# Optimization experiments

Hardware: AMD Instinct MI355X
Metric: run time of the kernel (lower is better)

## Reference

```python
import jax, jax.numpy as jnp
import numpy as np
from jax import lax

K = 3
K2 = K * K
EPS = 1e-5


def conv3x3(x, w, b=None):
    # x [B,C,H,W], w [O,C,3,3], padding=1, stride=1
    out = lax.conv_general_dilated(x, w, (1, 1), [(1, 1), (1, 1)],
                                   dimension_numbers=('NCHW', 'OIHW', 'NCHW'))
    if b is not None:
        out = out + b[None, :, None, None]
    return out


def deform_conv(x, w_off, b_off, w_mod, b_mod, w):
    # DCNv2-style deformable conv, k=3, stride=1, pad=1, dilation=1, no bias.
    B, C, H, W = x.shape
    O = w.shape[0]
    off = conv3x3(x, w_off, b_off).reshape(B, K2, 2, H, W)   # (dy,dx) per tap
    mod = 2.0 * jax.nn.sigmoid(conv3x3(x, w_mod, b_mod))      # [B,9,H,W]
    dy, dx = off[:, :, 0], off[:, :, 1]

    ky = (jnp.arange(K) - 1).astype(x.dtype)
    base_y = jnp.repeat(ky, K)   # [9]
    base_x = jnp.tile(ky, K)     # [9]
    ii = jnp.arange(H, dtype=x.dtype)[:, None]
    jj = jnp.arange(W, dtype=x.dtype)[None, :]
    py = ii[None, None] + base_y[None, :, None, None] + dy   # [B,9,H,W]
    px = jj[None, None] + base_x[None, :, None, None] + dx

    def sample(xb, pyb, pxb):
        # xb [C,H,W]; pyb/pxb [9,H,W] -> [C,9,H,W], bilinear w/ zero pad
        y0 = jnp.floor(pyb)
        x0 = jnp.floor(pxb)
        wy = pyb - y0
        wx = pxb - x0
        flat = xb.reshape(C, -1)
        acc = jnp.zeros((C, K2, H, W), xb.dtype)
        for yc, xc, wt in ((y0, x0, (1 - wy) * (1 - wx)),
                           (y0, x0 + 1, (1 - wy) * wx),
                           (y0 + 1, x0, wy * (1 - wx)),
                           (y0 + 1, x0 + 1, wy * wx)):
            yi = yc.astype(jnp.int32)
            xi = xc.astype(jnp.int32)
            valid = (yi >= 0) & (yi < H) & (xi >= 0) & (xi < W)
            idx = (jnp.clip(yi, 0, H - 1) * W + jnp.clip(xi, 0, W - 1)).reshape(-1)
            g = jnp.take(flat, idx, axis=1).reshape(C, K2, H, W)
            acc = acc + g * (wt * valid)[None]
        return acc

    patches = jax.vmap(sample)(x, py, px)          # [B,C,9,H,W]
    patches = patches * mod[:, None]               # modulated
    return jnp.einsum('bckhw,ock->bohw', patches, w.reshape(O, C, K2))


def bn_relu(x):
    # BatchNorm2d(affine=False), train-mode batch stats, biased variance
    mean = jnp.mean(x, axis=(0, 2, 3), keepdims=True)
    var = jnp.mean(jnp.square(x - mean), axis=(0, 2, 3), keepdims=True)
    return jax.nn.relu((x - mean) * lax.rsqrt(var + EPS))


def maxpool2(x):
    return lax.reduce_window(x, -jnp.inf, lax.max, (1, 1, 2, 2), (1, 1, 2, 2), 'VALID')


def setup_inputs() -> dict:
    key = jax.random.key(0)
    ks = jax.random.split(key, 11)
    B, Cin, Cout, H, W = 4, 64, 128, 128, 128
    std1 = 1.0 / np.sqrt(Cin * K2)
    std2 = 1.0 / np.sqrt(Cout * K2)
    return {
        'x': jax.random.normal(ks[0], (B, Cin, H, W), jnp.float32),
        'w_off1': jax.random.normal(ks[1], (2 * K2, Cin, K, K), jnp.float32) * 0.01,
        'b_off1': jax.random.normal(ks[2], (2 * K2,), jnp.float32) * 0.01,
        'w_mod1': jax.random.normal(ks[3], (K2, Cin, K, K), jnp.float32) * 0.01,
        'b_mod1': jnp.zeros((K2,), jnp.float32),
        'w1': jax.random.normal(ks[4], (Cout, Cin, K, K), jnp.float32) * std1,
        'w_off2': jax.random.normal(ks[5], (2 * K2, Cout, K, K), jnp.float32) * 0.01,
        'b_off2': jax.random.normal(ks[6], (2 * K2,), jnp.float32) * 0.01,
        'w_mod2': jax.random.normal(ks[7], (K2, Cout, K, K), jnp.float32) * 0.01,
        'b_mod2': jnp.zeros((K2,), jnp.float32),
        'w2': jax.random.normal(ks[8], (Cout, Cout, K, K), jnp.float32) * std2,
    }


def reference(x, w_off1, b_off1, w_mod1, b_mod1, w1,
              w_off2, b_off2, w_mod2, b_mod2, w2):
    h = bn_relu(deform_conv(x, w_off1, b_off1, w_mod1, b_mod1, w1))
    h = bn_relu(deform_conv(h, w_off2, b_off2, w_mod2, b_mod2, w2))
    return maxpool2(h)
```

## Files before the change

kernel.cpp:

```cpp
#include <hip/hip_runtime.h>
#include <math.h>

#define HH 128
#define WW 128
#define HWSZ 16384

typedef __attribute__((ext_vector_type(8))) _Float16 h8;
typedef __attribute__((ext_vector_type(2))) _Float16 h2;
typedef __attribute__((ext_vector_type(4))) float f32x4;
typedef __attribute__((ext_vector_type(2))) float f32x2;
typedef unsigned short ushort;

__device__ __forceinline__ ushort f2h(float f) {
    _Float16 h = (_Float16)f;
    ushort u;
    __builtin_memcpy(&u, &h, 2);
    return u;
}
__device__ __forceinline__ unsigned f2h2(float lo, float hi) {
    h2 r;
    r.x = (_Float16)lo;
    r.y = (_Float16)hi;
    unsigned u;
    __builtin_memcpy(&u, &r, 4);
    return u;
}
__device__ __forceinline__ f32x2 unpk_h2(unsigned u) {
    h2 h;
    __builtin_memcpy(&h, &u, 4);
    return (f32x2){(float)h.x, (float)h.y};
}

__global__ __launch_bounds__(256) void prep_weights(
    const float* __restrict__ w1, const float* __restrict__ w2,
    const float* __restrict__ w_off1, const float* __restrict__ w_mod1,
    const float* __restrict__ w_off2, const float* __restrict__ w_mod2,
    ushort* __restrict__ Wt1, ushort* __restrict__ Wt2,
    ushort* __restrict__ Wo1, ushort* __restrict__ Wo2) {
    int bid = blockIdx.x, tid = threadIdx.x;
    if (bid < 336) {
        int i = bid * 256 + tid;
        int o = i / 672, kq = i % 672;
        int k = kq / 72, c = kq % 72;
        float v = (k < 9 && c < 64) ? w1[(o * 64 + c) * 9 + k] : 0.f;
        Wt1[i] = f2h(v);
    } else if (bid < 960) {
        int i = (bid - 336) * 256 + tid;
        int o = i / 1248, kq = i % 1248;
        int k = kq / 136, c = kq % 136;
        float v = (k < 9 && c < 128) ? w2[(o * 128 + c) * 9 + k] : 0.f;
        Wt2[i] = f2h(v);
    } else if (bid < 1032) {
        int i = (bid - 960) * 256 + tid;
        int o = i / 576, kap = i % 576;
        int k = kap / 64, c = kap % 64;
        float v = 0.f;
        if (o < 18) v = w_off1[(o * 64 + c) * 9 + k];
        else if (o < 27) v = w_mod1[((o - 18) * 64 + c) * 9 + k];
        Wo1[i] = f2h(v);
    } else {
        int i = (bid - 1032) * 256 + tid;
        int o = i / 1152, kap = i % 1152;
        int k = kap / 128, c = kap % 128;
        float v = 0.f;
        if (o < 18) v = w_off2[(o * 128 + c) * 9 + k];
        else if (o < 27) v = w_mod2[((o - 18) * 128 + c) * 9 + k];
        Wo2[i] = f2h(v);
    }
}

template <int C>
__global__ __launch_bounds__(256) void nhwc_cvt(const float* __restrict__ xin,
                                                unsigned* __restrict__ xout) {
    __shared__ float tile[64][C + 1];
    const int m0 = blockIdx.x * 64;
    const int b = m0 >> 14;
    const int hw0 = m0 & 16383;
    const int t = threadIdx.x;
    const int pr = t & 63, cr = t >> 6;
#pragma unroll
    for (int it = 0; it < C / 4; ++it) {
        int c = it * 4 + cr;
        tile[pr][c] = xin[(((size_t)(b * C + c)) << 14) + hw0 + pr];
    }
    __syncthreads();
    constexpr int CH = C / 2;
#pragma unroll
    for (int it = 0; it < 64 * CH / 256; ++it) {
        int slot = it * 256 + t;
        int p = slot / CH, cc = slot % CH;
        xout[(size_t)(m0 + p) * CH + cc] =
            f2h2(tile[p][2 * cc], tile[p][2 * cc + 1]);
    }
}

__global__ __launch_bounds__(256) void bn_apply_ew(
    const unsigned* __restrict__ xin, const float* __restrict__ praw,
    unsigned* __restrict__ xout) {
    __shared__ float lstats[256];
    if (threadIdx.x < 128) {
        int c = threadIdx.x;
        float s = 0.f, q = 0.f;
#pragma unroll
        for (int r = 0; r < 8; ++r) {
            s += praw[r * 256 + c];
            q += praw[r * 256 + 128 + c];
        }
        float mean = s / 65536.f;
        float var = q / 65536.f - mean * mean;
        lstats[c] = mean;
        lstats[128 + c] = rsqrtf(var + 1e-5f);
    }
    __syncthreads();
    int i = blockIdx.x * 256 + threadIdx.x;
    uint4 v = ((const uint4*)xin)[i];
    int c0 = ((i * 4) & 63) * 2;
    unsigned ov[4];
    unsigned in[4] = {v.x, v.y, v.z, v.w};
#pragma unroll
    for (int d = 0; d < 4; ++d) {
        int c = c0 + 2 * d;
        f32x2 f = unpk_h2(in[d]);
        float a = fmaxf(0.f, (f.x - lstats[c]) * lstats[128 + c]);
        float b2 = fmaxf(0.f, (f.y - lstats[c + 1]) * lstats[128 + c + 1]);
        ov[d] = f2h2(a, b2);
    }
    ((uint4*)xout)[i] = uint4{ov[0], ov[1], ov[2], ov[3]};
}

template <int C>
__global__ __launch_bounds__(256) void offmod_nhwc(
    const ushort* __restrict__ xh, const ushort* __restrict__ wt,
    const float* __restrict__ b_off, const float* __restrict__ b_mod,
    float* __restrict__ dyb, float* __restrict__ dxb, float* __restrict__ mob,
    float* __restrict__ praw) {
    constexpr int K = C * 9;
    if (blockIdx.x < 8) praw[blockIdx.x * 256 + threadIdx.x] = 0.f;
    const int m0 = blockIdx.x * 64;
    const int b = m0 >> 14;
    const int hw0 = m0 & 16383;
    const int h = hw0 >> 7;
    const int w0 = hw0 & 127;
    const int tid = threadIdx.x;
    const int lane = tid & 63, wv = tid >> 6;
    const int n16 = lane & 15, quad = lane >> 4;
    const int p = wv * 16 + n16;
    const int w = w0 + p;

    int tbase[9];
    bool tval[9];
#pragma unroll
    for (int k = 0; k < 9; ++k) {
        int yy = h + k / 3 - 1, xx = w + k % 3 - 1;
        tval[k] = ((unsigned)yy < 128u) && ((unsigned)xx < 128u);
        int cy = min(max(yy, 0), 127), cx = min(max(xx, 0), 127);
        tbase[k] = ((b << 14) + (cy << 7) + cx) * C + quad * 8;
    }

    f32x4 acc[2];
    acc[0] = (f32x4){0.f, 0.f, 0.f, 0.f};
    acc[1] = (f32x4){0.f, 0.f, 0.f, 0.f};

    const ushort* b0p = wt + (size_t)n16 * K + quad * 8;
    const ushort* b1p = wt + (size_t)(16 + n16) * K + quad * 8;

#pragma unroll
    for (int s = 0; s < K / 32; ++s) {
        const int k = (s * 32) / C;
        const int c0 = (s * 32) % C;
        h8 a = {0, 0, 0, 0, 0, 0, 0, 0};
        if (tval[k]) a = *(const h8*)(xh + (size_t)tbase[k] + c0);
        const h8 bv0 = *(const h8*)(b0p + s * 32);
        const h8 bv1 = *(const h8*)(b1p + s * 32);
        acc[0] = __builtin_amdgcn_mfma_f32_16x16x32_f16(a, bv0, acc[0], 0, 0, 0);
        acc[1] = __builtin_amdgcn_mfma_f32_16x16x32_f16(a, bv1, acc[1], 0, 0, 0);
    }

    __shared__ float sm[32 * 65];
#pragma unroll
    for (int nt = 0; nt < 2; ++nt) {
        int n = nt * 16 + n16;
        int pb = wv * 16 + quad * 4;
#pragma unroll
        for (int r = 0; r < 4; ++r) sm[n * 65 + pb + r] = acc[nt][r];
    }
    __syncthreads();
    {
        int n = tid >> 3, i8 = tid & 7;
        if (n < 27) {
            const float* sp = sm + n * 65 + i8 * 8;
            int px = hw0 + i8 * 8;
            if (n < 18) {
                int k = n >> 1;
                float bias = b_off[n];
                float* dst =
                    ((n & 1) ? dxb : dyb) + (((size_t)(b * 9 + k)) << 14) + px;
#pragma unroll
                for (int j = 0; j < 8; j += 4) {
                    float4 v = make_float4(sp[j] + bias, sp[j + 1] + bias,
                                           sp[j + 2] + bias, sp[j + 3] + bias);
                    *(float4*)(dst + j) = v;
                }
            } else {
                float bias = b_mod[n - 18];
                float* dst = mob + (((size_t)(b * 9 + (n - 18))) << 14) + px;
#pragma unroll
                for (int j = 0; j < 8; j += 4) {
                    float4 v;
                    v.x = 2.f / (1.f + expf(-(sp[j] + bias)));
                    v.y = 2.f / (1.f + expf(-(sp[j + 1] + bias)));
                    v.z = 2.f / (1.f + expf(-(sp[j + 2] + bias)));
                    v.w = 2.f / (1.f + expf(-(sp[j + 3] + bias)));
                    *(float4*)(dst + j) = v;
                }
            }
        }
    }
}

template <int C>
__global__ __launch_bounds__(256, 4) void deform_mfma3(
    const ushort* __restrict__ xh, const float* __restrict__ dyb,
    const float* __restrict__ dxb, const float* __restrict__ mob,
    const ushort* __restrict__ wt, unsigned* __restrict__ xout,
    float* __restrict__ praw) {
    constexpr int PIX = 64;
    constexpr int NCH = C / 8;
    constexpr int NCC = C / 8;
    constexpr int NIT = PIX * NCC / 256;
    constexpr int HNIT = NIT / 2;
    constexpr int SH = (C / 32) / 2 > 0 ? (C / 32) / 2 : 1;
    constexpr int CPW = C + 8;
    constexpr int KP = ((9 * CPW + 31) / 32) * 32;
    constexpr int ABUF = PIX * C;
    constexpr int LOOPB = 2 * ABUF * 2 + PIX * 9 * 4 + PIX * 9 * 8;
    constexpr int EPIB = 128 * (PIX + 1) * 4;
    constexpr int SMEMB = LOOPB > EPIB ? LOOPB : EPIB;

    __shared__ __align__(16) char smem_raw[SMEMB];
    ushort* abuf0 = (ushort*)smem_raw;
    ushort* abuf1 = abuf0 + ABUF;
    int* tbl = (int*)(abuf0 + 2 * ABUF);
    unsigned* twl = (unsigned*)(smem_raw + 2 * ABUF * 2 + PIX * 9 * 4);

    const int m0 = blockIdx.x * PIX;
    const int b = m0 >> 14;
    const int hw0 = m0 & 16383;
    const int h = hw0 >> 7, w0 = hw0 & 127;
    const int tid = threadIdx.x;
    const int lane = tid & 63, wv = tid >> 6;
    const int n16 = lane & 15, quad = lane >> 4;
    const int xr = n16 & (NCH - 1);

    for (int r = tid; r < PIX * 9; r += 256) {
        int p = r & (PIX - 1), k = r >> 6;
        int oi = ((b * 9 + k) << 14) + hw0 + p;
        float py = (float)(h + k / 3 - 1) + dyb[oi];
        float px = (float)(w0 + p + k % 3 - 1) + dxb[oi];
        float mv = mob[oi];
        float y0f = floorf(py), x0f = floorf(px);
        float wy = py - y0f, wx = px - x0f;
        int y0 = (int)y0f, x0 = (int)x0f;
        int y1 = y0 + 1, x1 = x0 + 1;
        float f00 = (1.f - wy) * (1.f - wx) *
                    (((unsigned)y0 < 128u && (unsigned)x0 < 128u) ? mv : 0.f);
        float f01 = (1.f - wy) * wx *
                    (((unsigned)y0 < 128u && (unsigned)x1 < 128u) ? mv : 0.f);
        float f10 = wy * (1.f - wx) *
                    (((unsigned)y1 < 128u && (unsigned)x0 < 128u) ? mv : 0.f);
        float f11 = wy * wx *
                    (((unsigned)y1 < 128u && (unsigned)x1 < 128u) ? mv : 0.f);
        int cy0 = min(max(y0, 0), 127), cy1 = min(max(y1, 0), 127);
        int cx0 = min(max(x0, 0), 127), cx1 = min(max(x1, 0), 127);
        int base00 = (((b << 14) + (cy0 << 7) + cx0)) * C;
        int flags = ((cy1 != cy0) ? 2 : 0) | ((cx1 != cx0) ? 1 : 0);
        int s = p * 9 + k;
        tbl[s] = base00 | flags;
        twl[2 * s] = f2h2(f00, f01);
        twl[2 * s + 1] = f2h2(f10, f11);
    }
    __syncthreads();

    auto issue_loads = [&](int kc, int it0, uint4 (&q)[HNIT][4],
                           uint2 (&fw)[HNIT]) {
#pragma unroll
        for (int j = 0; j < HNIT; ++j) {
            int e = (it0 + j) * 256 + tid;
            int p = e / NCC, cc = e % NCC;
            int s = p * 9 + kc;
            int ent = tbl[s];
            fw[j] = *(const uint2*)&twl[2 * s];
            int base = ent & ~3;
            int dxo = (ent & 1) ? C : 0;
            int dyo = (ent & 2) ? (C << 7) : 0;
            const ushort* pp = xh + (size_t)base + cc * 8;
            q[j][0] = *(const uint4*)(pp);
            q[j][1] = *(const uint4*)(pp + dxo);
            q[j][2] = *(const uint4*)(pp + dyo);
            q[j][3] = *(const uint4*)(pp + dyo + dxo);
        }
    };
    auto interp_write = [&](ushort* dst, int it0, uint4 (&q)[HNIT][4],
                            uint2 (&fw)[HNIT]) {
#pragma unroll
        for (int j = 0; j < HNIT; ++j) {
            int e = (it0 + j) * 256 + tid;
            int p = e / NCC, cc = e % NCC;
            h2 w01, w23;
            __builtin_memcpy(&w01, &fw[j].x, 4);
            __builtin_memcpy(&w23, &fw[j].y, 4);
            h8 F0 = {w01.x, w01.x, w01.x, w01.x, w01.x, w01.x, w01.x, w01.x};
            h8 F1 = {w01.y, w01.y, w01.y, w01.y, w01.y, w01.y, w01.y, w01.y};
            h8 F2 = {w23.x, w23.x, w23.x, w23.x, w23.x, w23.x, w23.x, w23.x};
            h8 F3 = {w23.y, w23.y, w23.y, w23.y, w23.y, w23.y, w23.y, w23.y};
            h8 a0, a1, a2, a3;
            __builtin_memcpy(&a0, &q[j][0], 16);
            __builtin_memcpy(&a1, &q[j][1], 16);
            __builtin_memcpy(&a2, &q[j][2], 16);
            __builtin_memcpy(&a3, &q[j][3], 16);
            h8 v = a0 * F0 + a1 * F1 + a2 * F2 + a3 * F3;
            uint4 ov;
            __builtin_memcpy(&ov, &v, 16);
            int ccs = cc ^ (p & (NCH - 1));
            *(uint4*)&dst[p * C + ccs * 8] = ov;
        }
    };

    f32x4 acc[4][2];
#pragma unroll
    for (int mt = 0; mt < 4; ++mt)
#pragma unroll
        for (int nt = 0; nt < 2; ++nt) acc[mt][nt] = (f32x4){0.f, 0.f, 0.f, 0.f};

    const ushort* bbase[2];
#pragma unroll
    for (int nt = 0; nt < 2; ++nt)
        bbase[nt] = wt + (size_t)(wv * 32 + nt * 16 + n16) * KP + quad * 8;

    auto mfma_run = [&](const ushort* ab, int kc, int s0, int s1) {
#pragma unroll
        for (int s = s0; s < s1; ++s) {
            h8 av[4], bv[2];
            int ch = (s * 4 + quad) ^ xr;
#pragma unroll
            for (int mt = 0; mt < 4; ++mt)
                av[mt] = *(const h8*)(ab + (mt * 16 + n16) * C + ch * 8);
#pragma unroll
            for (int nt = 0; nt < 2; ++nt)
                bv[nt] = *(const h8*)(bbase[nt] + kc * CPW + s * 32);
#pragma unroll
            for (int mt = 0; mt < 4; ++mt)
#pragma unroll
                for (int nt = 0; nt < 2; ++nt)
                    acc[mt][nt] = __builtin_amdgcn_mfma_f32_16x16x32_f16(
                        av[mt], bv[nt], acc[mt][nt], 0, 0, 0);
        }
    };

    {
        uint4 q[HNIT][4];
        uint2 fw[HNIT];
        issue_loads(0, 0, q, fw);
        interp_write(abuf0, 0, q, fw);
        issue_loads(0, HNIT, q, fw);
        interp_write(abuf0, HNIT, q, fw);
    }
    __syncthreads();

#pragma unroll 1
    for (int kc = 0; kc < 9; ++kc) {
        const ushort* ab = (kc & 1) ? abuf1 : abuf0;
        ushort* dst = (kc & 1) ? abuf0 : abuf1;
        uint4 q[HNIT][4];
        uint2 fw[HNIT];
        if (kc < 8) issue_loads(kc + 1, 0, q, fw);
        mfma_run(ab, kc, 0, SH);
        if (kc < 8) {
            interp_write(dst, 0, q, fw);
            issue_loads(kc + 1, HNIT, q, fw);
        }
        mfma_run(ab, kc, SH, C / 32);
        if (kc < 8) interp_write(dst, HNIT, q, fw);
        __syncthreads();
    }

    float* sm = (float*)smem_raw;
    constexpr int SROW = PIX + 1;
#pragma unroll
    for (int mt = 0; mt < 4; ++mt)
#pragma unroll
        for (int nt = 0; nt < 2; ++nt) {
            int o = wv * 32 + nt * 16 + n16;
            int mb = mt * 16 + quad * 4;
#pragma unroll
            for (int r = 0; r < 4; ++r) sm[o * SROW + mb + r] = acc[mt][nt][r];
        }
    __syncthreads();
    {
        int o = tid >> 1, half = tid & 1;
        const float* sp = sm + o * SROW + half * 32;
        float s = 0.f, qq = 0.f;
#pragma unroll
        for (int i = 0; i < 32; i += 4) {
            float4 v = make_float4(sp[i], sp[i + 1], sp[i + 2], sp[i + 3]);
            s += v.x + v.y + v.z + v.w;
            qq += v.x * v.x + v.y * v.y + v.z * v.z + v.w * v.w;
        }
        s += __shfl_down(s, 1, 64);
        qq += __shfl_down(qq, 1, 64);
        if (half == 0) {
            float* pr = praw + (blockIdx.x & 7) * 256;
            atomicAdd(&pr[o], s);
            atomicAdd(&pr[128 + o], qq);
        }
    }
    {
        int p = tid >> 2, cc4 = tid & 3;
        unsigned ov[16];
#pragma unroll
        for (int j = 0; j < 16; ++j) {
            int c = cc4 * 32 + 2 * j;
            ov[j] = f2h2(sm[c * SROW + p], sm[(c + 1) * SROW + p]);
        }
        uint4* dst = (uint4*)(xout + ((size_t)(m0 + p)) * 64 + cc4 * 16);
        dst[0] = uint4{ov[0], ov[1], ov[2], ov[3]};
        dst[1] = uint4{ov[4], ov[5], ov[6], ov[7]};
        dst[2] = uint4{ov[8], ov[9], ov[10], ov[11]};
        dst[3] = uint4{ov[12], ov[13], ov[14], ov[15]};
    }
}

template <int C>
__global__ __launch_bounds__(256, 4) void deform_mfma3p(
    const ushort* __restrict__ xh, const float* __restrict__ dyb,
    const float* __restrict__ dxb, const float* __restrict__ mob,
    const ushort* __restrict__ wt, float* __restrict__ pout,
    float* __restrict__ praw) {
    constexpr int PIX = 64;
    constexpr int NCH = C / 8;
    constexpr int NCC = C / 8;
    constexpr int NIT = PIX * NCC / 256;
    constexpr int HNIT = NIT / 2;
    constexpr int SH = (C / 32) / 2 > 0 ? (C / 32) / 2 : 1;
    constexpr int CPW = C + 8;
    constexpr int KP = ((9 * CPW + 31) / 32) * 32;
    constexpr int ABUF = PIX * C;
    constexpr int LOOPB = 2 * ABUF * 2 + PIX * 9 * 4 + PIX * 9 * 8;
    constexpr int EPIB = 128 * (PIX + 1) * 4;
    constexpr int SMEMB = LOOPB > EPIB ? LOOPB : EPIB;

    __shared__ __align__(16) char smem_raw[SMEMB];
    ushort* abuf0 = (ushort*)smem_raw;
    ushort* abuf1 = abuf0 + ABUF;
    int* tbl = (int*)(abuf0 + 2 * ABUF);
    unsigned* twl = (unsigned*)(smem_raw + 2 * ABUF * 2 + PIX * 9 * 4);

    const int bid = blockIdx.x;
    const int b = bid >> 8;
    const int rp = (bid >> 2) & 63;
    const int g = bid & 3;
    const int tid = threadIdx.x;
    const int lane = tid & 63, wv = tid >> 6;
    const int n16 = lane & 15, quad = lane >> 4;
    const int xr = n16 & (NCH - 1);

    for (int r = tid; r < PIX * 9; r += 256) {
        int p = r & (PIX - 1), k = r >> 6;
        int row = 2 * rp + (p >> 5), col = g * 32 + (p & 31);
        int oi = ((b * 9 + k) << 14) + (row << 7) + col;
        float py = (float)(row + k / 3 - 1) + dyb[oi];
        float px = (float)(col + k % 3 - 1) + dxb[oi];
        float mv = mob[oi];
        float y0f = floorf(py), x0f = floorf(px);
        float wy = py - y0f, wx = px - x0f;
        int y0 = (int)y0f, x0 = (int)x0f;
        int y1 = y0 + 1, x1 = x0 + 1;
        float f00 = (1.f - wy) * (1.f - wx) *
                    (((unsigned)y0 < 128u && (unsigned)x0 < 128u) ? mv : 0.f);
        float f01 = (1.f - wy) * wx *
                    (((unsigned)y0 < 128u && (unsigned)x1 < 128u) ? mv : 0.f);
        float f10 = wy * (1.f - wx) *
                    (((unsigned)y1 < 128u && (unsigned)x0 < 128u) ? mv : 0.f);
        float f11 = wy * wx *
                    (((unsigned)y1 < 128u && (unsigned)x1 < 128u) ? mv : 0.f);
        int cy0 = min(max(y0, 0), 127), cy1 = min(max(y1, 0), 127);
        int cx0 = min(max(x0, 0), 127), cx1 = min(max(x1, 0), 127);
        int base00 = (((b << 14) + (cy0 << 7) + cx0)) * C;
        int flags = ((cy1 != cy0) ? 2 : 0) | ((cx1 != cx0) ? 1 : 0);
        int s = p * 9 + k;
        tbl[s] = base00 | flags;
        twl[2 * s] = f2h2(f00, f01);
        twl[2 * s + 1] = f2h2(f10, f11);
    }
    __syncthreads();

    auto issue_loads = [&](int kc, int it0, uint4 (&q)[HNIT][4],
                           uint2 (&fw)[HNIT]) {
#pragma unroll
        for (int j = 0; j < HNIT; ++j) {
            int e = (it0 + j) * 256 + tid;
            int p = e / NCC, cc = e % NCC;
            int s = p * 9 + kc;
            int ent = tbl[s];
            fw[j] = *(const uint2*)&twl[2 * s];
            int base = ent & ~3;
            int dxo = (ent & 1) ? C : 0;
            int dyo = (ent & 2) ? (C << 7) : 0;
            const ushort* pp = xh + (size_t)base + cc * 8;
            q[j][0] = *(const uint4*)(pp);
            q[j][1] = *(const uint4*)(pp + dxo);
            q[j][2] = *(const uint4*)(pp + dyo);
            q[j][3] = *(const uint4*)(pp + dyo + dxo);
        }
    };
    auto interp_write = [&](ushort* dst, int it0, uint4 (&q)[HNIT][4],
                            uint2 (&fw)[HNIT]) {
#pragma unroll
        for (int j = 0; j < HNIT; ++j) {
            int e = (it0 + j) * 256 + tid;
            int p = e / NCC, cc = e % NCC;
            h2 w01, w23;
            __builtin_memcpy(&w01, &fw[j].x, 4);
            __builtin_memcpy(&w23, &fw[j].y, 4);
            h8 F0 = {w01.x, w01.x, w01.x, w01.x, w01.x, w01.x, w01.x, w01.x};
            h8 F1 = {w01.y, w01.y, w01.y, w01.y, w01.y, w01.y, w01.y, w01.y};
            h8 F2 = {w23.x, w23.x, w23.x, w23.x, w23.x, w23.x, w23.x, w23.x};
            h8 F3 = {w23.y, w23.y, w23.y, w23.y, w23.y, w23.y, w23.y, w23.y};
            h8 a0, a1, a2, a3;
            __builtin_memcpy(&a0, &q[j][0], 16);
            __builtin_memcpy(&a1, &q[j][1], 16);
            __builtin_memcpy(&a2, &q[j][2], 16);
            __builtin_memcpy(&a3, &q[j][3], 16);
            h8 v = a0 * F0 + a1 * F1 + a2 * F2 + a3 * F3;
            uint4 ov;
            __builtin_memcpy(&ov, &v, 16);
            int ccs = cc ^ (p & (NCH - 1));
            *(uint4*)&dst[p * C + ccs * 8] = ov;
        }
    };

    f32x4 acc[4][2];
#pragma unroll
    for (int mt = 0; mt < 4; ++mt)
#pragma unroll
        for (int nt = 0; nt < 2; ++nt) acc[mt][nt] = (f32x4){0.f, 0.f, 0.f, 0.f};

    const ushort* bbase[2];
#pragma unroll
    for (int nt = 0; nt < 2; ++nt)
        bbase[nt] = wt + (size_t)(wv * 32 + nt * 16 + n16) * KP + quad * 8;

    auto mfma_run = [&](const ushort* ab, int kc, int s0, int s1) {
#pragma unroll
        for (int s = s0; s < s1; ++s) {
            h8 av[4], bv[2];
            int ch = (s * 4 + quad) ^ xr;
#pragma unroll
            for (int mt = 0; mt < 4; ++mt)
                av[mt] = *(const h8*)(ab + (mt * 16 + n16) * C + ch * 8);
#pragma unroll
            for (int nt = 0; nt < 2; ++nt)
                bv[nt] = *(const h8*)(bbase[nt] + kc * CPW + s * 32);
#pragma unroll
            for (int mt = 0; mt < 4; ++mt)
#pragma unroll
                for (int nt = 0; nt < 2; ++nt)
                    acc[mt][nt] = __builtin_amdgcn_mfma_f32_16x16x32_f16(
                        av[mt], bv[nt], acc[mt][nt], 0, 0, 0);
        }
    };

    {
        uint4 q[HNIT][4];
        uint2 fw[HNIT];
        issue_loads(0, 0, q, fw);
        interp_write(abuf0, 0, q, fw);
        issue_loads(0, HNIT, q, fw);
        interp_write(abuf0, HNIT, q, fw);
    }
    __syncthreads();

#pragma unroll 1
    for (int kc = 0; kc < 9; ++kc) {
        const ushort* ab = (kc & 1) ? abuf1 : abuf0;
        ushort* dst = (kc & 1) ? abuf0 : abuf1;
        uint4 q[HNIT][4];
        uint2 fw[HNIT];
        if (kc < 8) issue_loads(kc + 1, 0, q, fw);
        mfma_run(ab, kc, 0, SH);
        if (kc < 8) {
            interp_write(dst, 0, q, fw);
            issue_loads(kc + 1, HNIT, q, fw);
        }
        mfma_run(ab, kc, SH, C / 32);
        if (kc < 8) interp_write(dst, HNIT, q, fw);
        __syncthreads();
    }

    float* sm = (float*)smem_raw;
    constexpr int SROW = PIX + 1;
#pragma unroll
    for (int mt = 0; mt < 4; ++mt)
#pragma unroll
        for (int nt = 0; nt < 2; ++nt) {
            int o = wv * 32 + nt * 16 + n16;
            int mb = mt * 16 + quad * 4;
#pragma unroll
            for (int r = 0; r < 4; ++r) sm[o * SROW + mb + r] = acc[mt][nt][r];
        }
    __syncthreads();
    {
        int o = tid >> 1, half = tid & 1;
        const float* so = sm + o * SROW;
        const float* sp = so + half * 32;
        float s = 0.f, qq = 0.f;
#pragma unroll
        for (int i = 0; i < 32; i += 4) {
            float4 v = make_float4(sp[i], sp[i + 1], sp[i + 2], sp[i + 3]);
            s += v.x + v.y + v.z + v.w;
            qq += v.x * v.x + v.y * v.y + v.z * v.z + v.w * v.w;
        }
        s += __shfl_down(s, 1, 64);
        qq += __shfl_down(qq, 1, 64);
        if (half == 0) {
            float* pr = praw + (blockIdx.x & 7) * 256;
            atomicAdd(&pr[o], s);
            atomicAdd(&pr[128 + o], qq);
        }
        float4 pv0, pv1;
#pragma unroll
        for (int i = 0; i < 8; ++i) {
            int pc = half * 8 + i;
            float m0v = fmaxf(so[2 * pc], so[2 * pc + 1]);
            float m1v = fmaxf(so[32 + 2 * pc], so[32 + 2 * pc + 1]);
            float m = fmaxf(m0v, m1v);
            if (i < 4) ((float*)&pv0)[i] = m;
            else ((float*)&pv1)[i - 4] = m;
        }
        float* dp = pout + (((size_t)(b * 128 + o)) << 12) + rp * 64 + g * 16 +
                    half * 8;
        *(float4*)(dp) = pv0;
        *(float4*)(dp + 4) = pv1;
    }
}

__global__ __launch_bounds__(256) void pool_norm(const float* __restrict__ pout,
                                                 const float* __restrict__ praw,
                                                 float* __restrict__ out) {
    __shared__ float lstats[256];
    if (threadIdx.x < 128) {
        int c = threadIdx.x;
        float s = 0.f, q = 0.f;
#pragma unroll
        for (int r = 0; r < 8; ++r) {
            s += praw[r * 256 + c];
            q += praw[r * 256 + 128 + c];
        }
        float mean = s / 65536.f;
        float var = q / 65536.f - mean * mean;
        lstats[c] = mean;
        lstats[128 + c] = rsqrtf(var + 1e-5f);
    }
    __syncthreads();
    int i = blockIdx.x * 256 + threadIdx.x;
    int c = (i >> 10) & 127;
    float mean = lstats[c], rstd = lstats[128 + c];
    float4 v = ((const float4*)pout)[i];
    v.x = fmaxf(0.f, (v.x - mean) * rstd);
    v.y = fmaxf(0.f, (v.y - mean) * rstd);
    v.z = fmaxf(0.f, (v.z - mean) * rstd);
    v.w = fmaxf(0.f, (v.w - mean) * rstd);
    ((float4*)out)[i] = v;
}

extern "C" void kernel_launch(void* const* d_in, const int* in_sizes, int n_in,
                              void* d_out, int out_size, void* d_ws,
                              size_t ws_size, hipStream_t stream) {
    (void)in_sizes;
    (void)n_in;
    (void)out_size;
    (void)ws_size;
    const float* x = (const float*)d_in[0];
    const float* w_off1 = (const float*)d_in[1];
    const float* b_off1 = (const float*)d_in[2];
    const float* w_mod1 = (const float*)d_in[3];
    const float* b_mod1 = (const float*)d_in[4];
    const float* w1 = (const float*)d_in[5];
    const float* w_off2 = (const float*)d_in[6];
    const float* b_off2 = (const float*)d_in[7];
    const float* w_mod2 = (const float*)d_in[8];
    const float* b_mod2 = (const float*)d_in[9];
    const float* w2 = (const float*)d_in[10];
    float* out = (float*)d_out;
    float* ws = (float*)d_ws;

    ushort* Wt1 = (ushort*)ws;
    ushort* Wt2 = (ushort*)(ws + 43008);
    ushort* Wo1 = (ushort*)(ws + 43008 + 79872);
    ushort* Wo2 = (ushort*)(ws + 43008 + 79872 + 16384);
    float* dyb = ws + 172032;
    float* dxb = dyb + 589824;
    float* mob = dxb + 589824;
    float* hbuf = mob + 589824;
    float* xhf = hbuf + 8388608;
    float* h1hf = xhf + 2097152;
    float* praw = h1hf + 4194304;
    ushort* xh = (ushort*)xhf;
    ushort* h1h = (ushort*)h1hf;

    prep_weights<<<1176, 256, 0, stream>>>(w1, w2, w_off1, w_mod1, w_off2,
                                           w_mod2, Wt1, Wt2, Wo1, Wo2);

    nhwc_cvt<64><<<1024, 256, 0, stream>>>(x, (unsigned*)xh);
    offmod_nhwc<64><<<1024, 256, 0, stream>>>(xh, Wo1, b_off1, b_mod1, dyb, dxb,
                                              mob, praw);
    deform_mfma3<64><<<1024, 256, 0, stream>>>(xh, dyb, dxb, mob, Wt1,
                                               (unsigned*)hbuf, praw);
    bn_apply_ew<<<4096, 256, 0, stream>>>((const unsigned*)hbuf, praw,
                                          (unsigned*)h1h);

    offmod_nhwc<128><<<1024, 256, 0, stream>>>(h1h, Wo2, b_off2, b_mod2, dyb,
                                               dxb, mob, praw);
    deform_mfma3p<128><<<1024, 256, 0, stream>>>(h1h, dyb, dxb, mob, Wt2, hbuf,
                                                 praw);
    pool_norm<<<2048, 256, 0, stream>>>(hbuf, praw, out);
}
```

Measured before the change: 255.2 us.

## Issue all gather loads before MFMA, raise MFMA priority, swizzle block order

In both deformable-conv MFMA kernels, the split into half-batches of gather loads and half MFMA runs is replaced by one full batch of gather loads issued before the whole MFMA loop for the current tap, with interpolation written afterwards. The MFMA section is wrapped in s_setprio to favour matrix issue across waves. Block indices are remapped with an XCD-style stride-8 swizzle so adjacent blocks go to the same chiplet for L2 locality. Holding all NIT loads in flight raises register pressure and may cut occupancy under launch_bounds(256,4).

```diff
diff --git a/kernel.cpp b/kernel.cpp
--- a/kernel.cpp
+++ b/kernel.cpp
@@ -228,8 +228,6 @@
     constexpr int NCH = C / 8;
     constexpr int NCC = C / 8;
     constexpr int NIT = PIX * NCC / 256;
-    constexpr int HNIT = NIT / 2;
-    constexpr int SH = (C / 32) / 2 > 0 ? (C / 32) / 2 : 1;
     constexpr int CPW = C + 8;
     constexpr int KP = ((9 * CPW + 31) / 32) * 32;
     constexpr int ABUF = PIX * C;
@@ -243,7 +241,8 @@
     int* tbl = (int*)(abuf0 + 2 * ABUF);
     unsigned* twl = (unsigned*)(smem_raw + 2 * ABUF * 2 + PIX * 9 * 4);
 
-    const int m0 = blockIdx.x * PIX;
+    const int bid = (blockIdx.x & 7) * (gridDim.x >> 3) + (blockIdx.x >> 3);
+    const int m0 = bid * PIX;
     const int b = m0 >> 14;
     const int hw0 = m0 & 16383;
     const int h = hw0 >> 7, w0 = hw0 & 127;
@@ -281,11 +280,10 @@
     }
     __syncthreads();
 
-    auto issue_loads = [&](int kc, int it0, uint4 (&q)[HNIT][4],
-                           uint2 (&fw)[HNIT]) {
-#pragma unroll
-        for (int j = 0; j < HNIT; ++j) {
-            int e = (it0 + j) * 256 + tid;
+    auto issue_loads = [&](int kc, uint4 (&q)[NIT][4], uint2 (&fw)[NIT]) {
+#pragma unroll
+        for (int j = 0; j < NIT; ++j) {
+            int e = j * 256 + tid;
             int p = e / NCC, cc = e % NCC;
             int s = p * 9 + kc;
             int ent = tbl[s];
@@ -300,11 +298,10 @@
             q[j][3] = *(const uint4*)(pp + dyo + dxo);
         }
     };
-    auto interp_write = [&](ushort* dst, int it0, uint4 (&q)[HNIT][4],
-                            uint2 (&fw)[HNIT]) {
-#pragma unroll
-        for (int j = 0; j < HNIT; ++j) {
-            int e = (it0 + j) * 256 + tid;
+    auto interp_write = [&](ushort* dst, uint4 (&q)[NIT][4], uint2 (&fw)[NIT]) {
+#pragma unroll
+        for (int j = 0; j < NIT; ++j) {
+            int e = j * 256 + tid;
             int p = e / NCC, cc = e % NCC;
             h2 w01, w23;
             __builtin_memcpy(&w01, &fw[j].x, 4);
@@ -337,9 +334,9 @@
     for (int nt = 0; nt < 2; ++nt)
         bbase[nt] = wt + (size_t)(wv * 32 + nt * 16 + n16) * KP + quad * 8;
 
-    auto mfma_run = [&](const ushort* ab, int kc, int s0, int s1) {
-#pragma unroll
-        for (int s = s0; s < s1; ++s) {
+    auto mfma_run = [&](const ushort* ab, int kc) {
+#pragma unroll
+        for (int s = 0; s < C / 32; ++s) {
             h8 av[4], bv[2];
             int ch = (s * 4 + quad) ^ xr;
 #pragma unroll
@@ -358,12 +355,10 @@
     };
 
     {
-        uint4 q[HNIT][4];
-        uint2 fw[HNIT];
-        issue_loads(0, 0, q, fw);
-        interp_write(abuf0, 0, q, fw);
-        issue_loads(0, HNIT, q, fw);
-        interp_write(abuf0, HNIT, q, fw);
+        uint4 q[NIT][4];
+        uint2 fw[NIT];
+        issue_loads(0, q, fw);
+        interp_write(abuf0, q, fw);
     }
     __syncthreads();
 
@@ -371,16 +366,13 @@
     for (int kc = 0; kc < 9; ++kc) {
         const ushort* ab = (kc & 1) ? abuf1 : abuf0;
         ushort* dst = (kc & 1) ? abuf0 : abuf1;
-        uint4 q[HNIT][4];
-        uint2 fw[HNIT];
-        if (kc < 8) issue_loads(kc + 1, 0, q, fw);
-        mfma_run(ab, kc, 0, SH);
-        if (kc < 8) {
-            interp_write(dst, 0, q, fw);
-            issue_loads(kc + 1, HNIT, q, fw);
-        }
-        mfma_run(ab, kc, SH, C / 32);
-        if (kc < 8) interp_write(dst, HNIT, q, fw);
+        uint4 q[NIT][4];
+        uint2 fw[NIT];
+        if (kc < 8) issue_loads(kc + 1, q, fw);
+        __builtin_amdgcn_s_setprio(1);
+        mfma_run(ab, kc);
+        __builtin_amdgcn_s_setprio(0);
+        if (kc < 8) interp_write(dst, q, fw);
         __syncthreads();
     }
 
@@ -440,8 +432,6 @@
     constexpr int NCH = C / 8;
     constexpr int NCC = C / 8;
     constexpr int NIT = PIX * NCC / 256;
-    constexpr int HNIT = NIT / 2;
-    constexpr int SH = (C / 32) / 2 > 0 ? (C / 32) / 2 : 1;
     constexpr int CPW = C + 8;
     constexpr int KP = ((9 * CPW + 31) / 32) * 32;
     constexpr int ABUF = PIX * C;
@@ -455,7 +445,7 @@
     int* tbl = (int*)(abuf0 + 2 * ABUF);
     unsigned* twl = (unsigned*)(smem_raw + 2 * ABUF * 2 + PIX * 9 * 4);
 
-    const int bid = blockIdx.x;
+    const int bid = (blockIdx.x & 7) * (gridDim.x >> 3) + (blockIdx.x >> 3);
     const int b = bid >> 8;
     const int rp = (bid >> 2) & 63;
     const int g = bid & 3;
@@ -494,11 +484,10 @@
     }
     __syncthreads();
 
-    auto issue_loads = [&](int kc, int it0, uint4 (&q)[HNIT][4],
-                           uint2 (&fw)[HNIT]) {
-#pragma unroll
-        for (int j = 0; j < HNIT; ++j) {
-            int e = (it0 + j) * 256 + tid;
+    auto issue_loads = [&](int kc, uint4 (&q)[NIT][4], uint2 (&fw)[NIT]) {
+#pragma unroll
+        for (int j = 0; j < NIT; ++j) {
+            int e = j * 256 + tid;
             int p = e / NCC, cc = e % NCC;
             int s = p * 9 + kc;
             int ent = tbl[s];
@@ -513,11 +502,10 @@
             q[j][3] = *(const uint4*)(pp + dyo + dxo);
         }
     };
-    auto interp_write = [&](ushort* dst, int it0, uint4 (&q)[HNIT][4],
-                            uint2 (&fw)[HNIT]) {
-#pragma unroll
-        for (int j = 0; j < HNIT; ++j) {
-            int e = (it0 + j) * 256 + tid;
+    auto interp_write = [&](ushort* dst, uint4 (&q)[NIT][4], uint2 (&fw)[NIT]) {
+#pragma unroll
+        for (int j = 0; j < NIT; ++j) {
+            int e = j * 256 + tid;
             int p = e / NCC, cc = e % NCC;
             h2 w01, w23;
             __builtin_memcpy(&w01, &fw[j].x, 4);
@@ -550,9 +538,9 @@
     for (int nt = 0; nt < 2; ++nt)
         bbase[nt] = wt + (size_t)(wv * 32 + nt * 16 + n16) * KP + quad * 8;
 
-    auto mfma_run = [&](const ushort* ab, int kc, int s0, int s1) {
-#pragma unroll
-        for (int s = s0; s < s1; ++s) {
+    auto mfma_run = [&](const ushort* ab, int kc) {
+#pragma unroll
+        for (int s = 0; s < C / 32; ++s) {
             h8 av[4], bv[2];
             int ch = (s * 4 + quad) ^ xr;
 #pragma unroll
@@ -571,12 +559,10 @@
     };
 
     {
-        uint4 q[HNIT][4];
-        uint2 fw[HNIT];
-        issue_loads(0, 0, q, fw);
-        interp_write(abuf0, 0, q, fw);
-        issue_loads(0, HNIT, q, fw);
-        interp_write(abuf0, HNIT, q, fw);
+        uint4 q[NIT][4];
+        uint2 fw[NIT];
+        issue_loads(0, q, fw);
+        interp_write(abuf0, q, fw);
     }
     __syncthreads();
 
@@ -584,16 +570,13 @@
     for (int kc = 0; kc < 9; ++kc) {
         const ushort* ab = (kc & 1) ? abuf1 : abuf0;
         ushort* dst = (kc & 1) ? abuf0 : abuf1;
-        uint4 q[HNIT][4];
-        uint2 fw[HNIT];
-        if (kc < 8) issue_loads(kc + 1, 0, q, fw);
-        mfma_run(ab, kc, 0, SH);
-        if (kc < 8) {
-            interp_write(dst, 0, q, fw);
-            issue_loads(kc + 1, HNIT, q, fw);
-        }
-        mfma_run(ab, kc, SH, C / 32);
-        if (kc < 8) interp_write(dst, HNIT, q, fw);
+        uint4 q[NIT][4];
+        uint2 fw[NIT];
+        if (kc < 8) issue_loads(kc + 1, q, fw);
+        __builtin_amdgcn_s_setprio(1);
+        mfma_run(ab, kc);
+        __builtin_amdgcn_s_setprio(0);
+        if (kc < 8) interp_write(dst, q, fw);
         __syncthreads();
     }
 
```

Measured after the change: 276.9 us. 8.5% more time.
